# Performance work log

Hardware: AMD Instinct MI355X
Metric: run time of the kernel (lower is better)

Reference implementation:

```python
import jax, jax.numpy as jnp
import numpy as np

N, E, H, FN, FE, FO, L = 20000, 50000, 32, 4, 2, 4, 3

def _gelu(v):
    return jax.nn.gelu(v, approximate=False)  # torch nn.GELU default = exact erf

def setup_inputs() -> dict:
    key = jax.random.key(0)
    ks = jax.random.split(key, 24)
    def w(k, shape, fan_in):
        return jax.random.normal(k, shape, dtype=jnp.float32) / np.sqrt(fan_in)
    inp = {
        "x": jax.random.normal(ks[0], (N, FN), dtype=jnp.float32),
        "pred_mask": (jax.random.uniform(ks[1], (N, FN)) < 0.5).astype(jnp.float32),
        "edge_index": jax.random.randint(ks[2], (2, E), 0, N, dtype=jnp.int64),
        "edge_attr": jax.random.normal(ks[3], (E, FE), dtype=jnp.float32),
        # input encoder
        "W_in": w(ks[4], (FN, H), FN), "b_in": jnp.zeros((H,), jnp.float32),
        # mask embedding MLP
        "mW1": w(ks[5], (FN, H), FN), "mb1": jnp.zeros((H,), jnp.float32),
        "mW2": w(ks[6], (H, H), H),   "mb2": jnp.zeros((H,), jnp.float32),
        # per-layer stacked params (leading dim L)
        "eW1": w(ks[7], (L, FE, H), FE),    "eb1": jnp.zeros((L, H), jnp.float32),
        "eW2": w(ks[8], (L, H, H * H), H),  "eb2": jnp.zeros((L, H * H), jnp.float32),
        "W_root": w(ks[9], (L, H, H), H),   "conv_b": jnp.zeros((L, H), jnp.float32),
        "gamma": jnp.ones((L, H), jnp.float32), "beta": jnp.zeros((L, H), jnp.float32),
        # output decoder
        "dW1": w(ks[10], (H, H), H),  "db1": jnp.zeros((H,), jnp.float32),
        "dW2": w(ks[11], (H, FO), H), "db2": jnp.zeros((FO,), jnp.float32),
    }
    return inp

def reference(x, pred_mask, edge_index, edge_attr,
              W_in, b_in, mW1, mb1, mW2, mb2,
              eW1, eb1, eW2, eb2, W_root, conv_b, gamma, beta,
              dW1, db1, dW2, db2):
    # input projection + mask embedding
    h = x @ W_in + b_in + (_gelu(pred_mask @ mW1 + mb1) @ mW2 + mb2)
    # undirect graph (random edge list is directed -> torch path duplicates)
    src = jnp.concatenate([edge_index[0], edge_index[1]])  # [2E]
    dst = jnp.concatenate([edge_index[1], edge_index[0]])
    ea = jnp.concatenate([edge_attr, edge_attr], axis=0)    # [2E, FE]

    def layer(h, p):
        w1, b1, w2, b2, wr, cb, g, b = p
        # edge-conditioned weights: [2E, H, H]
        ew = (_gelu(ea @ w1 + b1) @ w2 + b2).reshape(-1, H, H)
        msg = jnp.einsum('eh,eho->eo', h[src], ew)          # gather + per-edge matvec
        agg = jax.ops.segment_sum(msg, dst, num_segments=N) # scatter-add
        hc = agg + h @ wr + cb                               # NNConv root weight + bias
        mu = jnp.mean(hc, axis=-1, keepdims=True)
        var = jnp.var(hc, axis=-1, keepdims=True)
        hn = (hc - mu) * jax.lax.rsqrt(var + 1e-5) * g + b   # LayerNorm
        return h + _gelu(hn), None                           # dropout in eval mode (no-op)

    h, _ = jax.lax.scan(layer, h, (eW1, eb1, eW2, eb2, W_root, conv_b, gamma, beta))
    out = _gelu(h @ dW1 + db1) @ dW2 + db2
    return out
```

## Files before the change

kernel.cpp:

```cpp
#include <hip/hip_runtime.h>
#include <hip/hip_bf16.h>
#include <math.h>

#define NN  20000
#define NE  50000
#define NE2 100000
#define H   32
#define FN  4
#define FE  2
#define FO  4
#define NL  3

#define FRAGS_PER_LAYER (33 * 2)
#define BVALS_PER_LAYER (FRAGS_PER_LAYER * 512)

typedef __attribute__((ext_vector_type(8))) short short8;
typedef __attribute__((ext_vector_type(4))) float f32x4;

__device__ __forceinline__ float gelu_f(float x) {
    return 0.5f * x * (1.0f + erff(x * 0.7071067811865476f));
}
__device__ __forceinline__ short f2bf(float x) {
    __hip_bfloat16 b = __float2bfloat16(x);
    return __builtin_bit_cast(short, b);
}
__device__ __forceinline__ float bf2f(short s) {
    __hip_bfloat16 b = __builtin_bit_cast(__hip_bfloat16, s);
    return __bfloat162float(b);
}

__global__ __launch_bounds__(256) void zero_agg(float4* __restrict__ p) {
    int i = blockIdx.x * 256 + threadIdx.x;
    if (i < NN * H / 4) p[i] = make_float4(0.f, 0.f, 0.f, 0.f);
}

__global__ __launch_bounds__(256) void prep_bfrag(
    const float* __restrict__ eW2, const float* __restrict__ eb2,
    short* __restrict__ Bhi, short* __restrict__ Blo)
{
    int idx = blockIdx.x * 256 + threadIdx.x;
    if (idx >= NL * BVALS_PER_LAYER) return;
    int layer = idx / BVALS_PER_LAYER;
    int rem   = idx - layer * BVALS_PER_LAYER;
    int f      = rem >> 9;
    int within = rem & 511;
    int step = f >> 1, nt = f & 1;
    int l = within >> 3, j = within & 7;
    int p = ((l >> 4) << 3) + j;
    int n = nt * 16 + (l & 15);
    float v;
    if (step < 32) v = eW2[layer * 32768 + step * 1024 + p * 32 + n];
    else           v = eb2[layer * 1024 + p * 32 + n];
    short hi = f2bf(v);
    short lo = f2bf(v - bf2f(hi));
    Bhi[idx] = hi;
    Blo[idx] = lo;
}

__global__ __launch_bounds__(256) void encoder(
    const float* __restrict__ x, const float* __restrict__ pm,
    const float* __restrict__ W_in, const float* __restrict__ b_in,
    const float* __restrict__ mW1, const float* __restrict__ mb1,
    const float* __restrict__ mW2, const float* __restrict__ mb2,
    float* __restrict__ h)
{
    __shared__ float sWin[FN*H], sW1[FN*H], sW2[H*H];
    __shared__ float sbin[H], sb1[H], sb2[H];
    int tid = threadIdx.x;
    for (int i = tid; i < FN*H; i += 256) { sWin[i] = W_in[i]; sW1[i] = mW1[i]; }
    for (int i = tid; i < H*H; i += 256) sW2[i] = mW2[i];
    if (tid < H) { sbin[tid] = b_in[tid]; sb1[tid] = mb1[tid]; sb2[tid] = mb2[tid]; }
    __syncthreads();
    int n = blockIdx.x * 256 + tid;
    if (n >= NN) return;
    float xv[FN], pv[FN];
#pragma unroll
    for (int i = 0; i < FN; ++i) { xv[i] = x[n*FN+i]; pv[i] = pm[n*FN+i]; }
    float m[H];
#pragma unroll
    for (int j = 0; j < H; ++j) {
        float a = sb1[j];
#pragma unroll
        for (int i = 0; i < FN; ++i) a += pv[i] * sW1[i*H+j];
        m[j] = gelu_f(a);
    }
#pragma unroll
    for (int j = 0; j < H; ++j) {
        float a = sbin[j] + sb2[j];
#pragma unroll
        for (int i = 0; i < FN; ++i) a += xv[i] * sWin[i*H+j];
        float s = 0.f;
#pragma unroll
        for (int k = 0; k < H; ++k) s += m[k] * sW2[k*H+j];
        h[n*H+j] = a + s;
    }
}

__global__ __launch_bounds__(64) void edge_pass(
    const float* __restrict__ h,
    const int* __restrict__ ei,
    const float* __restrict__ ea,
    const float* __restrict__ w1,
    const float* __restrict__ b1,
    const short* __restrict__ Bhi,
    const short* __restrict__ Blo,
    float* __restrict__ agg)
{
    __shared__ float t_lds[32 * 64];
    __shared__ int src_lds[64], dst_lds[64];

    int tid = threadIdx.x;
    int eb  = blockIdx.x * 64;
    {
        int e = eb + tid;
        bool v = e < NE2;
        int er = v ? (e < NE ? e : e - NE) : 0;
        int s, d;
        if (v && e >= NE) { s = ei[NE + er]; d = ei[er]; }
        else              { s = ei[er];      d = ei[NE + er]; }
        if (!v) { s = 0; d = 0; }
        src_lds[tid] = s; dst_lds[tid] = d;
        float a0 = v ? ea[er*2]   : 0.f;
        float a1 = v ? ea[er*2+1] : 0.f;
        for (int k = 0; k < 32; ++k) {
            float tv = v ? gelu_f(a0 * w1[k] + a1 * w1[32+k] + b1[k]) : 0.f;
            t_lds[k*64 + tid] = tv;
        }
    }
    __syncthreads();

    int lg = tid >> 4, lm = tid & 15;

    float hs[4][8];
#pragma unroll
    for (int m = 0; m < 4; ++m) {
        int s = src_lds[m*16 + lm];
        const float4* hp = (const float4*)(h + s*H + lg*8);
        float4 u0 = hp[0], u1 = hp[1];
        hs[m][0]=u0.x; hs[m][1]=u0.y; hs[m][2]=u0.z; hs[m][3]=u0.w;
        hs[m][4]=u1.x; hs[m][5]=u1.y; hs[m][6]=u1.z; hs[m][7]=u1.w;
    }

    f32x4 acc[4][2];
#pragma unroll
    for (int m = 0; m < 4; ++m) {
        acc[m][0] = (f32x4){0.f,0.f,0.f,0.f};
        acc[m][1] = (f32x4){0.f,0.f,0.f,0.f};
    }

    const short8* Bh = (const short8*)Bhi;
    const short8* Bl = (const short8*)Blo;
    short8 cb0h = Bh[tid], cb1h = Bh[64 + tid];
    short8 cb0l = Bl[tid], cb1l = Bl[64 + tid];
    short8 nb0h = cb0h, nb1h = cb1h, nb0l = cb0l, nb1l = cb1l;

#pragma unroll 1
    for (int step = 0; step < 33; ++step) {
        if (step < 32) {
            int fo = (step + 1) * 128 + tid;
            nb0h = Bh[fo]; nb1h = Bh[fo + 64];
            nb0l = Bl[fo]; nb1l = Bl[fo + 64];
        }
#pragma unroll
        for (int m = 0; m < 4; ++m) {
            float tv = (step < 32) ? t_lds[step*64 + m*16 + lm] : 1.0f;
            short8 a;
#pragma unroll
            for (int j = 0; j < 8; ++j) a[j] = f2bf(tv * hs[m][j]);
            acc[m][0] = __builtin_amdgcn_mfma_f32_16x16x32_bf16(a, cb0h, acc[m][0], 0, 0, 0);
            acc[m][0] = __builtin_amdgcn_mfma_f32_16x16x32_bf16(a, cb0l, acc[m][0], 0, 0, 0);
            acc[m][1] = __builtin_amdgcn_mfma_f32_16x16x32_bf16(a, cb1h, acc[m][1], 0, 0, 0);
            acc[m][1] = __builtin_amdgcn_mfma_f32_16x16x32_bf16(a, cb1l, acc[m][1], 0, 0, 0);
        }
        cb0h = nb0h; cb1h = nb1h; cb0l = nb0l; cb1l = nb1l;
    }

#pragma unroll
    for (int m = 0; m < 4; ++m) {
#pragma unroll
        for (int r = 0; r < 4; ++r) {
            int erow = m*16 + lg*4 + r;
            if (eb + erow < NE2) {
                int d = dst_lds[erow];
                atomicAdd(agg + d*H + lm,      acc[m][0][r]);
                atomicAdd(agg + d*H + 16 + lm, acc[m][1][r]);
            }
        }
    }
}

__global__ __launch_bounds__(256) void node_update(
    float* __restrict__ h, const float* __restrict__ agg,
    const float* __restrict__ wr, const float* __restrict__ cb,
    const float* __restrict__ gamma, const float* __restrict__ beta)
{
    __shared__ float swr[H*H];
    __shared__ float scb[H], sg[H], sb[H];
    int tid = threadIdx.x;
    for (int i = tid; i < H*H; i += 256) swr[i] = wr[i];
    if (tid < H) { scb[tid] = cb[tid]; sg[tid] = gamma[tid]; sb[tid] = beta[tid]; }
    __syncthreads();
    int n = blockIdx.x * 256 + tid;
    if (n >= NN) return;

    float hv[H], hc[H];
#pragma unroll
    for (int q = 0; q < 8; ++q) {
        float4 v = ((const float4*)(h + n*H))[q];
        hv[q*4+0]=v.x; hv[q*4+1]=v.y; hv[q*4+2]=v.z; hv[q*4+3]=v.w;
        float4 g = ((const float4*)(agg + n*H))[q];
        hc[q*4+0]=g.x; hc[q*4+1]=g.y; hc[q*4+2]=g.z; hc[q*4+3]=g.w;
    }
#pragma unroll
    for (int o = 0; o < H; ++o) hc[o] += scb[o];
#pragma unroll
    for (int k = 0; k < H; ++k) {
        float hk = hv[k];
#pragma unroll
        for (int o = 0; o < H; ++o) hc[o] += hk * swr[k*H+o];
    }
    float mu = 0.f;
#pragma unroll
    for (int o = 0; o < H; ++o) mu += hc[o];
    mu *= (1.0f/H);
    float var = 0.f;
#pragma unroll
    for (int o = 0; o < H; ++o) { float d = hc[o]-mu; var += d*d; }
    var *= (1.0f/H);
    float rs = rsqrtf(var + 1e-5f);
#pragma unroll
    for (int o = 0; o < H; ++o) {
        float hn = (hc[o]-mu)*rs*sg[o] + sb[o];
        hv[o] += gelu_f(hn);
    }
#pragma unroll
    for (int q = 0; q < 8; ++q) {
        float4 v = make_float4(hv[q*4+0], hv[q*4+1], hv[q*4+2], hv[q*4+3]);
        ((float4*)(h + n*H))[q] = v;
    }
}

__global__ __launch_bounds__(256) void decoder(
    const float* __restrict__ h,
    const float* __restrict__ dW1, const float* __restrict__ db1,
    const float* __restrict__ dW2, const float* __restrict__ db2,
    float* __restrict__ out)
{
    __shared__ float sW1[H*H], sW2[H*FO];
    __shared__ float sb1[H], sb2[FO];
    int tid = threadIdx.x;
    for (int i = tid; i < H*H; i += 256) sW1[i] = dW1[i];
    for (int i = tid; i < H*FO; i += 256) sW2[i] = dW2[i];
    if (tid < H) sb1[tid] = db1[tid];
    if (tid < FO) sb2[tid] = db2[tid];
    __syncthreads();
    int n = blockIdx.x * 256 + tid;
    if (n >= NN) return;
    float hv[H];
#pragma unroll
    for (int q = 0; q < 8; ++q) {
        float4 v = ((const float4*)(h + n*H))[q];
        hv[q*4+0]=v.x; hv[q*4+1]=v.y; hv[q*4+2]=v.z; hv[q*4+3]=v.w;
    }
    float g[H];
#pragma unroll
    for (int j = 0; j < H; ++j) {
        float a = sb1[j];
#pragma unroll
        for (int k = 0; k < H; ++k) a += hv[k] * sW1[k*H+j];
        g[j] = gelu_f(a);
    }
#pragma unroll
    for (int o = 0; o < FO; ++o) {
        float a = sb2[o];
#pragma unroll
        for (int k = 0; k < H; ++k) a += g[k] * sW2[k*FO+o];
        out[n*FO+o] = a;
    }
}

extern "C" void kernel_launch(void* const* d_in, const int* in_sizes, int n_in,
                              void* d_out, int out_size, void* d_ws, size_t ws_size,
                              hipStream_t stream)
{
    const float* x    = (const float*)d_in[0];
    const float* pm   = (const float*)d_in[1];
    const int*   ei   = (const int*)d_in[2];
    const float* ea   = (const float*)d_in[3];
    const float* W_in = (const float*)d_in[4];
    const float* b_in = (const float*)d_in[5];
    const float* mW1  = (const float*)d_in[6];
    const float* mb1  = (const float*)d_in[7];
    const float* mW2  = (const float*)d_in[8];
    const float* mb2  = (const float*)d_in[9];
    const float* eW1  = (const float*)d_in[10];
    const float* eb1  = (const float*)d_in[11];
    const float* eW2  = (const float*)d_in[12];
    const float* eb2  = (const float*)d_in[13];
    const float* Wr   = (const float*)d_in[14];
    const float* cb   = (const float*)d_in[15];
    const float* gm   = (const float*)d_in[16];
    const float* bt   = (const float*)d_in[17];
    const float* dW1  = (const float*)d_in[18];
    const float* db1  = (const float*)d_in[19];
    const float* dW2  = (const float*)d_in[20];
    const float* db2  = (const float*)d_in[21];
    float* out = (float*)d_out;

    float* h   = (float*)d_ws;
    float* agg = h + NN*H;
    short* Bhi = (short*)(agg + NN*H);
    short* Blo = Bhi + NL * BVALS_PER_LAYER;

    prep_bfrag<<<(NL*BVALS_PER_LAYER + 255)/256, 256, 0, stream>>>(eW2, eb2, Bhi, Blo);
    encoder<<<(NN + 255)/256, 256, 0, stream>>>(x, pm, W_in, b_in, mW1, mb1, mW2, mb2, h);

    for (int l = 0; l < NL; ++l) {
        zero_agg<<<(NN*H/4 + 255)/256, 256, 0, stream>>>((float4*)agg);
        edge_pass<<<(NE2 + 63)/64, 64, 0, stream>>>(
            h, ei, ea, eW1 + l*FE*H, eb1 + l*H,
            Bhi + l*BVALS_PER_LAYER, Blo + l*BVALS_PER_LAYER, agg);
        node_update<<<(NN + 255)/256, 256, 0, stream>>>(
            h, agg, Wr + l*H*H, cb + l*H, gm + l*H, bt + l*H);
    }

    decoder<<<(NN + 255)/256, 256, 0, stream>>>(h, dW1, db1, dW2, db2, out);
}
```

Baseline: 187.2 us.

## Precompute edge MLP activations for all layers and fuse setup, zeroing, decoder kernels

```diff
diff --git a/kernel.cpp b/kernel.cpp
--- a/kernel.cpp
+++ b/kernel.cpp
@@ -14,6 +14,12 @@
 #define FRAGS_PER_LAYER (33 * 2)
 #define BVALS_PER_LAYER (FRAGS_PER_LAYER * 512)
 
+#define TCHUNKS 196
+#define NB_TALL (NL * 32 * TCHUNKS)
+#define NB_PREP ((NL * BVALS_PER_LAYER + 255)/256)
+#define NB_ZERO (NN * H / 4 / 256)
+#define NB_ENC  ((NN + 255)/256)
+
 typedef __attribute__((ext_vector_type(8))) short short8;
 typedef __attribute__((ext_vector_type(4))) float f32x4;
 
@@ -29,49 +35,74 @@
     return __bfloat162float(b);
 }
 
-__global__ __launch_bounds__(256) void zero_agg(float4* __restrict__ p) {
-    int i = blockIdx.x * 256 + threadIdx.x;
-    if (i < NN * H / 4) p[i] = make_float4(0.f, 0.f, 0.f, 0.f);
-}
-
-__global__ __launch_bounds__(256) void prep_bfrag(
-    const float* __restrict__ eW2, const float* __restrict__ eb2,
-    short* __restrict__ Bhi, short* __restrict__ Blo)
-{
-    int idx = blockIdx.x * 256 + threadIdx.x;
-    if (idx >= NL * BVALS_PER_LAYER) return;
-    int layer = idx / BVALS_PER_LAYER;
-    int rem   = idx - layer * BVALS_PER_LAYER;
-    int f      = rem >> 9;
-    int within = rem & 511;
-    int step = f >> 1, nt = f & 1;
-    int l = within >> 3, j = within & 7;
-    int p = ((l >> 4) << 3) + j;
-    int n = nt * 16 + (l & 15);
-    float v;
-    if (step < 32) v = eW2[layer * 32768 + step * 1024 + p * 32 + n];
-    else           v = eb2[layer * 1024 + p * 32 + n];
-    short hi = f2bf(v);
-    short lo = f2bf(v - bf2f(hi));
-    Bhi[idx] = hi;
-    Blo[idx] = lo;
-}
-
-__global__ __launch_bounds__(256) void encoder(
+__global__ __launch_bounds__(256) void prologue(
     const float* __restrict__ x, const float* __restrict__ pm,
     const float* __restrict__ W_in, const float* __restrict__ b_in,
     const float* __restrict__ mW1, const float* __restrict__ mb1,
     const float* __restrict__ mW2, const float* __restrict__ mb2,
-    float* __restrict__ h)
+    const float* __restrict__ eW1, const float* __restrict__ eb1,
+    const float* __restrict__ eW2, const float* __restrict__ eb2,
+    const float* __restrict__ ea,
+    float* __restrict__ h, float* __restrict__ agg,
+    short* __restrict__ Bhi, short* __restrict__ Blo,
+    float* __restrict__ tfull)
 {
+    int bid = blockIdx.x;
+    int tid = threadIdx.x;
+
+    if (bid < NB_TALL) {
+        int l     = bid / (32 * TCHUNKS);
+        int rem   = bid - l * 32 * TCHUNKS;
+        int k     = rem / TCHUNKS;
+        int chunk = rem - k * TCHUNKS;
+        int er    = chunk * 256 + tid;
+        float w0 = eW1[l*FE*H + k];
+        float w1 = eW1[l*FE*H + H + k];
+        float bb = eb1[l*H + k];
+        if (er < NE) {
+            float tv = gelu_f(ea[er*2] * w0 + ea[er*2+1] * w1 + bb);
+            tfull[(l*32 + k) * NE + er] = tv;
+        }
+        return;
+    }
+    bid -= NB_TALL;
+
+    if (bid < NB_PREP) {
+        int idx = bid * 256 + tid;
+        if (idx >= NL * BVALS_PER_LAYER) return;
+        int layer = idx / BVALS_PER_LAYER;
+        int rem   = idx - layer * BVALS_PER_LAYER;
+        int f      = rem >> 9;
+        int within = rem & 511;
+        int step = f >> 1, nt = f & 1;
+        int l = within >> 3, j = within & 7;
+        int p = ((l >> 4) << 3) + j;
+        int n = nt * 16 + (l & 15);
+        float v;
+        if (step < 32) v = eW2[layer * 32768 + step * 1024 + p * 32 + n];
+        else           v = eb2[layer * 1024 + p * 32 + n];
+        short hi = f2bf(v);
+        short lo = f2bf(v - bf2f(hi));
+        Bhi[idx] = hi;
+        Blo[idx] = lo;
+        return;
+    }
+    bid -= NB_PREP;
+
+    if (bid < NB_ZERO) {
+        int i = bid * 256 + tid;
+        ((float4*)agg)[i] = make_float4(0.f, 0.f, 0.f, 0.f);
+        return;
+    }
+    bid -= NB_ZERO;
+
     __shared__ float sWin[FN*H], sW1[FN*H], sW2[H*H];
     __shared__ float sbin[H], sb1[H], sb2[H];
-    int tid = threadIdx.x;
     for (int i = tid; i < FN*H; i += 256) { sWin[i] = W_in[i]; sW1[i] = mW1[i]; }
     for (int i = tid; i < H*H; i += 256) sW2[i] = mW2[i];
     if (tid < H) { sbin[tid] = b_in[tid]; sb1[tid] = mb1[tid]; sb2[tid] = mb2[tid]; }
     __syncthreads();
-    int n = blockIdx.x * 256 + tid;
+    int n = bid * 256 + tid;
     if (n >= NN) return;
     float xv[FN], pv[FN];
 #pragma unroll
@@ -96,45 +127,54 @@
     }
 }
 
-__global__ __launch_bounds__(64) void edge_pass(
+__global__ __launch_bounds__(256) void edge_pass(
     const float* __restrict__ h,
     const int* __restrict__ ei,
-    const float* __restrict__ ea,
-    const float* __restrict__ w1,
-    const float* __restrict__ b1,
+    const float* __restrict__ tfull_l,
     const short* __restrict__ Bhi,
     const short* __restrict__ Blo,
     float* __restrict__ agg)
 {
-    __shared__ float t_lds[32 * 64];
-    __shared__ int src_lds[64], dst_lds[64];
+    __shared__ float t_lds[32][256];
+    __shared__ int src_lds[256], dst_lds[256];
 
     int tid = threadIdx.x;
-    int eb  = blockIdx.x * 64;
+    int bid = blockIdx.x;
+    bool half2 = bid >= TCHUNKS;
+    int er_base = (half2 ? bid - TCHUNKS : bid) * 256;
+
     {
-        int e = eb + tid;
-        bool v = e < NE2;
-        int er = v ? (e < NE ? e : e - NE) : 0;
+        int er = er_base + tid;
+        int erc = er < NE ? er : NE - 1;
         int s, d;
-        if (v && e >= NE) { s = ei[NE + er]; d = ei[er]; }
-        else              { s = ei[er];      d = ei[NE + er]; }
-        if (!v) { s = 0; d = 0; }
-        src_lds[tid] = s; dst_lds[tid] = d;
-        float a0 = v ? ea[er*2]   : 0.f;
-        float a1 = v ? ea[er*2+1] : 0.f;
-        for (int k = 0; k < 32; ++k) {
-            float tv = v ? gelu_f(a0 * w1[k] + a1 * w1[32+k] + b1[k]) : 0.f;
-            t_lds[k*64 + tid] = tv;
+        if (half2) { s = ei[NE + erc]; d = ei[erc]; }
+        else       { s = ei[erc];      d = ei[NE + erc]; }
+        bool v = er < NE;
+        src_lds[tid] = v ? s : 0;
+        dst_lds[tid] = v ? d : 0;
+    }
+    {
+        int c  = tid & 63;
+        int kq = tid >> 6;
+        int col = er_base + c * 4;
+        if (col > NE - 4) col = NE - 4;
+#pragma unroll
+        for (int q = 0; q < 8; ++q) {
+            int k = q * 4 + kq;
+            float4 tv = *(const float4*)(tfull_l + k * NE + col);
+            *(float4*)&t_lds[k][c * 4] = tv;
         }
     }
     __syncthreads();
 
-    int lg = tid >> 4, lm = tid & 15;
+    int wv = tid >> 6, lane = tid & 63;
+    int lg = lane >> 4, lm = lane & 15;
+    int jbase = wv * 64;
 
     float hs[4][8];
 #pragma unroll
     for (int m = 0; m < 4; ++m) {
-        int s = src_lds[m*16 + lm];
+        int s = src_lds[jbase + m*16 + lm];
         const float4* hp = (const float4*)(h + s*H + lg*8);
         float4 u0 = hp[0], u1 = hp[1];
         hs[m][0]=u0.x; hs[m][1]=u0.y; hs[m][2]=u0.z; hs[m][3]=u0.w;
@@ -150,20 +190,20 @@
 
     const short8* Bh = (const short8*)Bhi;
     const short8* Bl = (const short8*)Blo;
-    short8 cb0h = Bh[tid], cb1h = Bh[64 + tid];
-    short8 cb0l = Bl[tid], cb1l = Bl[64 + tid];
+    short8 cb0h = Bh[lane], cb1h = Bh[64 + lane];
+    short8 cb0l = Bl[lane], cb1l = Bl[64 + lane];
     short8 nb0h = cb0h, nb1h = cb1h, nb0l = cb0l, nb1l = cb1l;
 
 #pragma unroll 1
     for (int step = 0; step < 33; ++step) {
         if (step < 32) {
-            int fo = (step + 1) * 128 + tid;
+            int fo = (step + 1) * 128 + lane;
             nb0h = Bh[fo]; nb1h = Bh[fo + 64];
             nb0l = Bl[fo]; nb1l = Bl[fo + 64];
         }
 #pragma unroll
         for (int m = 0; m < 4; ++m) {
-            float tv = (step < 32) ? t_lds[step*64 + m*16 + lm] : 1.0f;
+            float tv = (step < 32) ? t_lds[step][jbase + m*16 + lm] : 1.0f;
             short8 a;
 #pragma unroll
             for (int j = 0; j < 8; ++j) a[j] = f2bf(tv * hs[m][j]);
@@ -179,8 +219,8 @@
     for (int m = 0; m < 4; ++m) {
 #pragma unroll
         for (int r = 0; r < 4; ++r) {
-            int erow = m*16 + lg*4 + r;
-            if (eb + erow < NE2) {
+            int erow = jbase + m*16 + lg*4 + r;
+            if (er_base + erow < NE) {
                 int d = dst_lds[erow];
                 atomicAdd(agg + d*H + lm,      acc[m][0][r]);
                 atomicAdd(agg + d*H + 16 + lm, acc[m][1][r]);
@@ -190,15 +230,20 @@
 }
 
 __global__ __launch_bounds__(256) void node_update(
-    float* __restrict__ h, const float* __restrict__ agg,
+    float* __restrict__ h, float* __restrict__ agg,
     const float* __restrict__ wr, const float* __restrict__ cb,
-    const float* __restrict__ gamma, const float* __restrict__ beta)
+    const float* __restrict__ gamma, const float* __restrict__ beta,
+    const float* __restrict__ dW1, const float* __restrict__ db1,
+    const float* __restrict__ dW2, const float* __restrict__ db2,
+    float* __restrict__ out, int last)
 {
-    __shared__ float swr[H*H];
-    __shared__ float scb[H], sg[H], sb[H];
+    __shared__ float swr[H*H], sW1d[H*H], sW2d[H*FO];
+    __shared__ float scb[H], sg[H], sb[H], sb1d[H], sb2d[FO];
     int tid = threadIdx.x;
-    for (int i = tid; i < H*H; i += 256) swr[i] = wr[i];
-    if (tid < H) { scb[tid] = cb[tid]; sg[tid] = gamma[tid]; sb[tid] = beta[tid]; }
+    for (int i = tid; i < H*H; i += 256) { swr[i] = wr[i]; sW1d[i] = dW1[i]; }
+    for (int i = tid; i < H*FO; i += 256) sW2d[i] = dW2[i];
+    if (tid < H) { scb[tid] = cb[tid]; sg[tid] = gamma[tid]; sb[tid] = beta[tid]; sb1d[tid] = db1[tid]; }
+    if (tid < FO) sb2d[tid] = db2[tid];
     __syncthreads();
     int n = blockIdx.x * 256 + tid;
     if (n >= NN) return;
@@ -233,49 +278,29 @@
         float hn = (hc[o]-mu)*rs*sg[o] + sb[o];
         hv[o] += gelu_f(hn);
     }
-#pragma unroll
-    for (int q = 0; q < 8; ++q) {
-        float4 v = make_float4(hv[q*4+0], hv[q*4+1], hv[q*4+2], hv[q*4+3]);
-        ((float4*)(h + n*H))[q] = v;
-    }
-}
-
-__global__ __launch_bounds__(256) void decoder(
-    const float* __restrict__ h,
-    const float* __restrict__ dW1, const float* __restrict__ db1,
-    const float* __restrict__ dW2, const float* __restrict__ db2,
-    float* __restrict__ out)
-{
-    __shared__ float sW1[H*H], sW2[H*FO];
-    __shared__ float sb1[H], sb2[FO];
-    int tid = threadIdx.x;
-    for (int i = tid; i < H*H; i += 256) sW1[i] = dW1[i];
-    for (int i = tid; i < H*FO; i += 256) sW2[i] = dW2[i];
-    if (tid < H) sb1[tid] = db1[tid];
-    if (tid < FO) sb2[tid] = db2[tid];
-    __syncthreads();
-    int n = blockIdx.x * 256 + tid;
-    if (n >= NN) return;
-    float hv[H];
-#pragma unroll
-    for (int q = 0; q < 8; ++q) {
-        float4 v = ((const float4*)(h + n*H))[q];
-        hv[q*4+0]=v.x; hv[q*4+1]=v.y; hv[q*4+2]=v.z; hv[q*4+3]=v.w;
-    }
-    float g[H];
-#pragma unroll
-    for (int j = 0; j < H; ++j) {
-        float a = sb1[j];
-#pragma unroll
-        for (int k = 0; k < H; ++k) a += hv[k] * sW1[k*H+j];
-        g[j] = gelu_f(a);
-    }
-#pragma unroll
-    for (int o = 0; o < FO; ++o) {
-        float a = sb2[o];
-#pragma unroll
-        for (int k = 0; k < H; ++k) a += g[k] * sW2[k*FO+o];
-        out[n*FO+o] = a;
+
+    if (!last) {
+#pragma unroll
+        for (int q = 0; q < 8; ++q) {
+            ((float4*)(h + n*H))[q]   = make_float4(hv[q*4+0], hv[q*4+1], hv[q*4+2], hv[q*4+3]);
+            ((float4*)(agg + n*H))[q] = make_float4(0.f, 0.f, 0.f, 0.f);
+        }
+    } else {
+        float g[H];
+#pragma unroll
+        for (int j = 0; j < H; ++j) {
+            float a = sb1d[j];
+#pragma unroll
+            for (int k = 0; k < H; ++k) a += hv[k] * sW1d[k*H+j];
+            g[j] = gelu_f(a);
+        }
+#pragma unroll
+        for (int o = 0; o < FO; ++o) {
+            float a = sb2d[o];
+#pragma unroll
+            for (int k = 0; k < H; ++k) a += g[k] * sW2d[k*FO+o];
+            out[n*FO+o] = a;
+        }
     }
 }
 
@@ -307,22 +332,22 @@
     const float* db2  = (const float*)d_in[21];
     float* out = (float*)d_out;
 
-    float* h   = (float*)d_ws;
-    float* agg = h + NN*H;
-    short* Bhi = (short*)(agg + NN*H);
-    short* Blo = Bhi + NL * BVALS_PER_LAYER;
-
-    prep_bfrag<<<(NL*BVALS_PER_LAYER + 255)/256, 256, 0, stream>>>(eW2, eb2, Bhi, Blo);
-    encoder<<<(NN + 255)/256, 256, 0, stream>>>(x, pm, W_in, b_in, mW1, mb1, mW2, mb2, h);
+    float* h     = (float*)d_ws;
+    float* agg   = h + NN*H;
+    float* tfull = agg + NN*H;
+    short* Bhi   = (short*)(tfull + NL*32*NE);
+    short* Blo   = Bhi + NL * BVALS_PER_LAYER;
+
+    prologue<<<NB_TALL + NB_PREP + NB_ZERO + NB_ENC, 256, 0, stream>>>(
+        x, pm, W_in, b_in, mW1, mb1, mW2, mb2, eW1, eb1, eW2, eb2, ea,
+        h, agg, Bhi, Blo, tfull);
 
     for (int l = 0; l < NL; ++l) {
-        zero_agg<<<(NN*H/4 + 255)/256, 256, 0, stream>>>((float4*)agg);
-        edge_pass<<<(NE2 + 63)/64, 64, 0, stream>>>(
-            h, ei, ea, eW1 + l*FE*H, eb1 + l*H,
+        edge_pass<<<2*TCHUNKS, 256, 0, stream>>>(
+            h, ei, tfull + l*32*NE,
             Bhi + l*BVALS_PER_LAYER, Blo + l*BVALS_PER_LAYER, agg);
         node_update<<<(NN + 255)/256, 256, 0, stream>>>(
-            h, agg, Wr + l*H*H, cb + l*H, gm + l*H, bt + l*H);
-    }
-
-    decoder<<<(NN + 255)/256, 256, 0, stream>>>(h, dW1, db1, dW2, db2, out);
-}
+            h, agg, Wr + l*H*H, cb + l*H, gm + l*H, bt + l*H,
+            dW1, db1, dW2, db2, out, l == NL-1);
+    }
+}
```

After: 181.1 us. -3.3%, faster.
